# Performance work log

Measured on AMD Instinct MI355X. Metric: run time of the kernel, lower is better.

Reference implementation:

```python
import jax, jax.numpy as jnp
import numpy as np

N_HEADS = 8; DH = 64; G = 4; K = 9
C = N_HEADS * DH; CG = C // G
FACTOR = 2.0; TAU = 1.0
SCALE = DH ** -0.5


def _conv1x1(x, w, b):
    # x: (C, *spatial), w: (O, C), b: (O,)
    y = jnp.tensordot(w, x, axes=([1], [0]))
    return y + b.reshape((-1,) + (1,) * (y.ndim - 1))


def _dwconv(x, w, b):
    # depthwise 3x3, SAME padding; x (N,Cg,H,W), w (Cg,1,3,3)
    y = jax.lax.conv_general_dilated(x, w, (1, 1), 'SAME',
                                     feature_group_count=x.shape[1],
                                     dimension_numbers=('NCHW', 'OIHW', 'NCHW'))
    return y + b[None, :, None, None]


def _ln(x, g, b):
    # LayerNormProxy: LN over channel dim of NCHW (torch default eps=1e-5)
    m = jnp.mean(x, axis=1, keepdims=True)
    v = jnp.var(x, axis=1, keepdims=True)
    return (x - m) / jnp.sqrt(v + 1e-5) * g[None, :, None, None] + b[None, :, None, None]


def _grid_sample(img, grid):
    # bilinear, align_corners=True, padding_mode='zeros'
    # img (N,C,H,W), grid (N,Hg,Wg,2) with (x,y) in [-1,1]
    N, Cc, H, W = img.shape
    gx = (grid[..., 0] + 1.0) * 0.5 * (W - 1)
    gy = (grid[..., 1] + 1.0) * 0.5 * (H - 1)
    x0 = jnp.floor(gx); y0 = jnp.floor(gy)

    def g(yy, xx):
        yi = jnp.clip(yy, 0, H - 1).astype(jnp.int32)
        xi = jnp.clip(xx, 0, W - 1).astype(jnp.int32)
        ok = ((yy >= 0) & (yy <= H - 1) & (xx >= 0) & (xx <= W - 1)).astype(img.dtype)
        vals = jax.vmap(lambda im, a, b: im[:, a, b])(img, yi, xi)  # (N,C,Hg,Wg)
        return vals * ok[:, None]

    wx1 = gx - x0; wx0 = 1.0 - wx1
    wy1 = gy - y0; wy0 = 1.0 - wy1
    return (g(y0, x0) * (wy0 * wx0)[:, None]
            + g(y0, x0 + 1) * (wy0 * wx1)[:, None]
            + g(y0 + 1, x0) * (wy1 * wx0)[:, None]
            + g(y0 + 1, x0 + 1) * (wy1 * wx1)[:, None])


def _forward(x, idx, labels, wq, bq, wk, bk, wv, bv, wo, bo,
             ow1, ob1, g1, b1, ow2, ob2, g2, b2, ow3):
    _, _, H, W = x.shape
    n = idx.shape[0]
    iy, ix = idx[:, 0], idx[:, 1]

    q = _conv1x1(x[0], wq, bq)[None]               # (1,C,H,W)
    q_off = q.reshape(G, CG, H, W)                 # (b g) c h w with b=1
    q_sel = q[0][:, iy, ix]                        # (C,n)

    # offset predictor: dwconv -> LN -> GELU (x2) -> 1x1 (no bias)
    t = jax.nn.gelu(_ln(_dwconv(q_off, ow1, ob1), g1, b1), approximate=False)
    t = jax.nn.gelu(_ln(_dwconv(t, ow2, ob2), g2, b2), approximate=False)
    offset = jnp.einsum('gchw,oc->gohw', t, ow3)   # (G,2K,H,W)

    # offset_range_factor > 0: tanh * [1/H,1/W] (tiled K times) * factor
    rng = jnp.tile(jnp.array([1.0 / H, 1.0 / W], offset.dtype), K)
    offset = jnp.tanh(offset) * rng[None, :, None, None] * FACTOR
    off = offset.transpose(0, 2, 3, 1).reshape(G, H, W, K, 2)  # (g,h,w,K,(y,x))

    # reference points in [-1,1] (y,x), unfolded over 3x3 window w/ replication pad
    ry = (jnp.arange(H, dtype=x.dtype) + 0.5) / H * 2.0 - 1.0
    rx = (jnp.arange(W, dtype=x.dtype) + 0.5) / W * 2.0 - 1.0
    ref = jnp.stack(jnp.meshgrid(ry, rx, indexing='ij'), 0)    # (2,H,W)
    pad = jnp.pad(ref, ((0, 0), (1, 1), (1, 1)), mode='edge')
    patches = jnp.stack([pad[:, dy:dy + H, dx:dx + W]
                         for dy in range(3) for dx in range(3)], 0)  # (K,2,H,W)
    ref_unf = patches.transpose(2, 3, 0, 1)                    # (H,W,K,2)

    pos = off + ref_unf[None]                                  # (G,H,W,K,2)
    pos = pos.transpose(0, 3, 1, 2, 4).reshape(G * K, H, W, 2)
    grid = pos[..., ::-1]                                      # (x,y) order

    # gather per-group channels at K learned locations per position
    xg = x.reshape(G, CG, H, W)
    img = jnp.broadcast_to(xg[:, None], (G, K, CG, H, W)).reshape(G * K, CG, H, W)
    xs = _grid_sample(img, grid)                               # (GK,CG,H,W)
    xs = xs.reshape(G, K, CG, H, W).transpose(0, 2, 1, 3, 4).reshape(C, K, H, W)
    xs_sel = xs[:, :, iy, ix]                                  # (C,K,n)

    k = _conv1x1(xs_sel, wk, bk).reshape(N_HEADS, DH, K, n).transpose(0, 1, 3, 2)  # (h,d,n,K)
    v = _conv1x1(xs_sel, wv, bv).reshape(N_HEADS, DH, K, n).transpose(0, 1, 3, 2)
    qh = q_sel.reshape(N_HEADS, DH, n)

    attn = jnp.einsum('hdn,hdnk->hnk', qh, k) * SCALE
    attn = jax.nn.softmax(attn / TAU, axis=-1)                 # (h,n,K)
    out = jnp.einsum('hnk,hdnk->hdn', attn, v).reshape(C, n)
    y = _conv1x1(out, wo, bo).T                                # (n, dim_out)

    sig = jax.nn.sigmoid(y[jnp.arange(n), labels])

    # second grid_sample over full channels at the same learned positions
    img_full = jnp.broadcast_to(x, (G * K, C, H, W))
    xr = _grid_sample(img_full, grid)                          # (GK,C,H,W)
    xr_sel = xr[:, :, iy, ix].transpose(2, 0, 1)               # (n,GK,C)
    return y, attn, xr_sel, sig


def setup_inputs() -> dict:
    key = jax.random.key(0)
    ks = jax.random.split(key, 16)
    H = W = 64; n = 2048; s = 0.02
    return dict(
        x=jax.random.normal(ks[0], (1, C, H, W), jnp.float32),
        idx=jax.random.randint(ks[1], (n, 2), 0, H),
        labels=jax.random.randint(ks[2], (n,), 0, C),
        wq=jax.random.normal(ks[3], (C, C), jnp.float32) * s, bq=jnp.zeros((C,), jnp.float32),
        wk=jax.random.normal(ks[4], (C, C), jnp.float32) * s, bk=jnp.zeros((C,), jnp.float32),
        wv=jax.random.normal(ks[5], (C, C), jnp.float32) * s, bv=jnp.zeros((C,), jnp.float32),
        wo=jax.random.normal(ks[6], (C, C), jnp.float32) * s, bo=jnp.zeros((C,), jnp.float32),
        ow1=jax.random.normal(ks[7], (CG, 1, 3, 3), jnp.float32) * s, ob1=jnp.zeros((CG,), jnp.float32),
        g1=jnp.ones((CG,), jnp.float32), b1=jnp.zeros((CG,), jnp.float32),
        ow2=jax.random.normal(ks[8], (CG, 1, 3, 3), jnp.float32) * s, ob2=jnp.zeros((CG,), jnp.float32),
        g2=jnp.ones((CG,), jnp.float32), b2=jnp.zeros((CG,), jnp.float32),
        ow3=jax.random.normal(ks[9], (2 * K, CG), jnp.float32) * s,
    )


def reference(x, idx, labels, wq, bq, wk, bk, wv, bv, wo, bo,
              ow1, ob1, g1, b1, ow2, ob2, g2, b2, ow3):
    return _forward(x, idx, labels, wq, bq, wk, bk, wv, bv, wo, bo,
                    ow1, ob1, g1, b1, ow2, ob2, g2, b2, ow3)
```

## Files before the change

### kernel.cpp

```cpp
#include <hip/hip_runtime.h>
#include <math.h>

namespace {

typedef unsigned short u16;
typedef unsigned int u32;
typedef __attribute__((ext_vector_type(8))) short bf16x8;
typedef __attribute__((ext_vector_type(4))) float f32x4;
typedef __attribute__((ext_vector_type(2))) float f32x2;
typedef __attribute__((ext_vector_type(2))) unsigned int u32x2;

constexpr int HDIM = 64;
constexpr int WDIM = 64;
constexpr int HW = HDIM * WDIM;
constexpr int C = 512;
constexpr int G = 4;
constexpr int CG = 128;
constexpr int K = 9;
constexpr int NH = 8;
constexpr float SCALE = 0.125f;

__device__ __forceinline__ u16 f2b(float f) {
  union { float f; u32 u; } v; v.f = f;
  u32 u = v.u;
  return (u16)((u + 0x7FFFu + ((u >> 16) & 1u)) >> 16);
}
__device__ __forceinline__ float b2f(u16 b) {
  union { u32 u; float f; } v; v.u = ((u32)b) << 16;
  return v.f;
}

__global__ void __launch_bounds__(256)
k_prep(const float* __restrict__ wq, const float* __restrict__ wv,
       const float* __restrict__ wo, const float* __restrict__ wk,
       const float* __restrict__ x,
       u16* __restrict__ wqb, u16* __restrict__ wvb, u16* __restrict__ wob,
       u16* __restrict__ wkT, u16* __restrict__ xtb) {
  int b = blockIdx.x;
  int t = threadIdx.x;
  if (b < 1024) {
    int j = b * 256 + t;
    wqb[j] = f2b(wq[j]);
    wvb[j] = f2b(wv[j]);
    wob[j] = f2b(wo[j]);
    return;
  }
  __shared__ float tile[32][33];
  int tx = t & 31, ty = t >> 5;
  if (b < 1280) {
    int bb = b - 1024;
    int r0 = (bb & 15) * 32, c0 = (bb >> 4) * 32;
    for (int r = ty; r < 32; r += 8) tile[r][tx] = wk[(r0 + r) * C + c0 + tx];
    __syncthreads();
    for (int r = ty; r < 32; r += 8) wkT[(c0 + r) * C + r0 + tx] = f2b(tile[tx][r]);
  } else {
    int bb = b - 1280;
    int p0 = (bb & 127) * 32, c0 = (bb >> 7) * 32;
    for (int r = ty; r < 32; r += 8) tile[r][tx] = x[(c0 + r) * HW + p0 + tx];
    __syncthreads();
    for (int r = ty; r < 32; r += 8) xtb[(p0 + r) * C + c0 + tx] = f2b(tile[tx][r]);
  }
}

template <bool OUT_BF16>
__global__ void __launch_bounds__(256)
k_gemm_mfma(const u16* __restrict__ A, int lda, int aOffZ,
            const int* __restrict__ aIdx,
            const u16* __restrict__ BT, int ldb, int bOffZ,
            const float* __restrict__ bias, int biasOffZ,
            void* __restrict__ Dp, int ldd, int dOffZ, int Kd,
            const int* __restrict__ labels, float* __restrict__ sigp) {
  int z = blockIdx.z;
  const u16* Ab = A + (size_t)z * aOffZ;
  const u16* Bb = BT + (size_t)z * bOffZ;
  int t = threadIdx.x;
  int wave = t >> 6, lane = t & 63;
  int wm = (wave >> 1) * 32, wn = (wave & 1) * 32;
  int bm = blockIdx.x * 64 + wm;
  int bn = blockIdx.y * 64 + wn;
  int row = lane & 15, quad = lane >> 4;
  size_t ar[2];
#pragma unroll
  for (int mt = 0; mt < 2; ++mt) {
    int r = bm + mt * 16 + row;
    ar[mt] = aIdx ? (size_t)(aIdx[2 * r] * WDIM + aIdx[2 * r + 1]) : (size_t)r;
  }
  f32x4 acc[2][2] = {};
  for (int k0 = 0; k0 < Kd; k0 += 32) {
    bf16x8 a[2], b[2];
#pragma unroll
    for (int mt = 0; mt < 2; ++mt)
      a[mt] = *(const bf16x8*)&Ab[ar[mt] * lda + k0 + quad * 8];
#pragma unroll
    for (int nt = 0; nt < 2; ++nt)
      b[nt] = *(const bf16x8*)&Bb[(size_t)(bn + nt * 16 + row) * ldb + k0 + quad * 8];
#pragma unroll
    for (int mt = 0; mt < 2; ++mt)
#pragma unroll
      for (int nt = 0; nt < 2; ++nt)
        acc[mt][nt] = __builtin_amdgcn_mfma_f32_16x16x32_bf16(a[mt], b[nt], acc[mt][nt], 0, 0, 0);
  }
#pragma unroll
  for (int nt = 0; nt < 2; ++nt) {
    int cc = bn + nt * 16 + row;
    float bb = bias ? bias[(size_t)z * biasOffZ + cc] : 0.0f;
#pragma unroll
    for (int mt = 0; mt < 2; ++mt)
#pragma unroll
      for (int r = 0; r < 4; ++r) {
        int rr = bm + mt * 16 + quad * 4 + r;
        float v = acc[mt][nt][r] + bb;
        if (OUT_BF16) {
          ((u16*)Dp)[(size_t)z * dOffZ + (size_t)rr * ldd + cc] = f2b(v);
        } else {
          ((float*)Dp)[(size_t)z * dOffZ + (size_t)rr * ldd + cc] = v;
          if (labels && labels[rr] == cc) sigp[rr] = 1.0f / (1.0f + expf(-v));
        }
      }
  }
}

__global__ void __launch_bounds__(256)
k_dwln2(const u16* __restrict__ in, const float* __restrict__ w9,
        const float* __restrict__ wb, const float* __restrict__ lng,
        const float* __restrict__ lnb, u16* __restrict__ outp) {
  int p = blockIdx.x;
  int h = p >> 6, w = p & 63;
  int t = threadIdx.x;
  int c0 = t * 2;
  int cg0 = c0 & 127, cg1 = cg0 + 1;
  float a0 = wb[cg0], a1 = wb[cg1];
#pragma unroll
  for (int dy = 0; dy < 3; ++dy) {
    int hh = h + dy - 1;
    if (hh < 0 || hh >= HDIM) continue;
#pragma unroll
    for (int dx = 0; dx < 3; ++dx) {
      int ww = w + dx - 1;
      if (ww < 0 || ww >= WDIM) continue;
      u32 pr2 = *(const u32*)&in[(hh * WDIM + ww) * C + c0];
      float wt0 = w9[cg0 * 9 + dy * 3 + dx];
      float wt1 = w9[cg1 * 9 + dy * 3 + dx];
      a0 += wt0 * b2f((u16)pr2);
      a1 += wt1 * b2f((u16)(pr2 >> 16));
    }
  }
  float s = a0 + a1, s2 = a0 * a0 + a1 * a1;
#pragma unroll
  for (int o = 32; o > 0; o >>= 1) {
    s += __shfl_xor(s, o, 64);
    s2 += __shfl_xor(s2, o, 64);
  }
  float mean = s * (1.0f / 128.0f);
  float var = s2 * (1.0f / 128.0f) - mean * mean;
  float rstd = rsqrtf(var + 1e-5f);
  float xn0 = (a0 - mean) * rstd * lng[cg0] + lnb[cg0];
  float xn1 = (a1 - mean) * rstd * lng[cg1] + lnb[cg1];
  u16 o0 = f2b(0.5f * xn0 * (1.0f + erff(xn0 * 0.70710678f)));
  u16 o1 = f2b(0.5f * xn1 * (1.0f + erff(xn1 * 0.70710678f)));
  *(u32*)&outp[(size_t)p * C + c0] = ((u32)o1 << 16) | o0;
}

__global__ void __launch_bounds__(256)
k_dwoff(const u16* __restrict__ t1, const float* __restrict__ w9,
        const float* __restrict__ wb, const float* __restrict__ lng,
        const float* __restrict__ lnb, const float* __restrict__ ow3,
        const int* __restrict__ idx, float* __restrict__ pos) {
  int i = blockIdx.x;
  int t = threadIdx.x;
  int iy = idx[2 * i], ix = idx[2 * i + 1];
  int c0 = t * 2;
  int cg0 = c0 & 127, cg1 = cg0 + 1;
  int g = t >> 6;
  int lane = t & 63;
  float a0 = wb[cg0], a1 = wb[cg1];
#pragma unroll
  for (int dy = 0; dy < 3; ++dy) {
    int hh = iy + dy - 1;
    if (hh < 0 || hh >= HDIM) continue;
#pragma unroll
    for (int dx = 0; dx < 3; ++dx) {
      int ww = ix + dx - 1;
      if (ww < 0 || ww >= WDIM) continue;
      u32 pr2 = *(const u32*)&t1[(hh * WDIM + ww) * C + c0];
      float wt0 = w9[cg0 * 9 + dy * 3 + dx];
      float wt1 = w9[cg1 * 9 + dy * 3 + dx];
      a0 += wt0 * b2f((u16)pr2);
      a1 += wt1 * b2f((u16)(pr2 >> 16));
    }
  }
  float s = a0 + a1, s2 = a0 * a0 + a1 * a1;
#pragma unroll
  for (int o = 32; o > 0; o >>= 1) {
    s += __shfl_xor(s, o, 64);
    s2 += __shfl_xor(s2, o, 64);
  }
  float mean = s * (1.0f / 128.0f);
  float var = s2 * (1.0f / 128.0f) - mean * mean;
  float rstd = rsqrtf(var + 1e-5f);
  float xn0 = (a0 - mean) * rstd * lng[cg0] + lnb[cg0];
  float xn1 = (a1 - mean) * rstd * lng[cg1] + lnb[cg1];
  float x0 = 0.5f * xn0 * (1.0f + erff(xn0 * 0.70710678f));
  float x1 = 0.5f * xn1 * (1.0f + erff(xn1 * 0.70710678f));
  float ovreg = 0.0f;
#pragma unroll
  for (int l = 0; l < 18; ++l) {
    float a = ow3[l * CG + cg0] * x0 + ow3[l * CG + cg1] * x1;
#pragma unroll
    for (int o = 32; o > 0; o >>= 1) a += __shfl_xor(a, o, 64);
    if (lane == l) ovreg = a;
  }
  int ls = (lane < 9) ? lane : 0;
  float vy = __shfl(ovreg, 2 * ls, 64);
  float vx = __shfl(ovreg, 2 * ls + 1, 64);
  if (lane < 9) {
    int dy = lane / 3, dx = lane % 3;
    int ryi = min(max(iy + dy - 1, 0), HDIM - 1);
    int rxi = min(max(ix + dx - 1, 0), WDIM - 1);
    float ry = (ryi + 0.5f) * (2.0f / HDIM) - 1.0f;
    float rx = (rxi + 0.5f) * (2.0f / WDIM) - 1.0f;
    f32x2 pv;
    pv.x = tanhf(vy) * (2.0f / HDIM) + ry;
    pv.y = tanhf(vx) * (2.0f / WDIM) + rx;
    *(f32x2*)&pos[((i * G + g) * K + lane) * 2] = pv;
  }
}

__global__ void __launch_bounds__(256)
k_attn3(const u16* __restrict__ qk2b, const u16* __restrict__ xtb,
        const float* __restrict__ pos, float* __restrict__ attn_out,
        u16* __restrict__ z2b, float* __restrict__ xr, int n) {
  constexpr int LD = 520;
  int i = blockIdx.x;
  int t = threadIdx.x;
  __shared__ alignas(16) u16 qkl[8 * LD];
  __shared__ alignas(16) u16 xsl[16 * LD];
  __shared__ int ro[36][4];
  __shared__ float wbl[36][4];
  __shared__ float lg[NH][K];
  __shared__ float pr[NH][K];
  {
    const bf16x8* qs = (const bf16x8*)(qk2b + (size_t)i * (NH * C));
#pragma unroll
    for (int cix = t; cix < 512; cix += 256) {
      bf16x8 val = qs[cix];
      int r = cix >> 6;
      int co = (cix & 63) * 8;
      *(bf16x8*)&qkl[r * LD + co] = val;
    }
  }
  if (t < 36) {
    float py = pos[(size_t)i * 72 + 2 * t];
    float px = pos[(size_t)i * 72 + 2 * t + 1];
    float gx = (px + 1.0f) * 0.5f * (WDIM - 1);
    float gy = (py + 1.0f) * 0.5f * (HDIM - 1);
    float x0f = floorf(gx), y0f = floorf(gy);
    float wx1 = gx - x0f, wx0 = 1.0f - wx1;
    float wy1 = gy - y0f, wy0 = 1.0f - wy1;
    int x0 = (int)x0f, y0 = (int)y0f;
    int x1 = x0 + 1, y1 = y0 + 1;
    bool vx0 = (x0 >= 0) && (x0 < WDIM);
    bool vx1 = (x1 >= 0) && (x1 < WDIM);
    bool vy0 = (y0 >= 0) && (y0 < HDIM);
    bool vy1 = (y1 >= 0) && (y1 < HDIM);
    wbl[t][0] = (vy0 && vx0) ? wy0 * wx0 : 0.0f;
    wbl[t][1] = (vy0 && vx1) ? wy0 * wx1 : 0.0f;
    wbl[t][2] = (vy1 && vx0) ? wy1 * wx0 : 0.0f;
    wbl[t][3] = (vy1 && vx1) ? wy1 * wx1 : 0.0f;
    int x0c = min(max(x0, 0), WDIM - 1), x1c = min(max(x1, 0), WDIM - 1);
    int y0c = min(max(y0, 0), HDIM - 1), y1c = min(max(y1, 0), HDIM - 1);
    ro[t][0] = (y0c * WDIM + x0c) * C;
    ro[t][1] = (y0c * WDIM + x1c) * C;
    ro[t][2] = (y1c * WDIM + x0c) * C;
    ro[t][3] = (y1c * WDIM + x1c) * C;
  }
  __syncthreads();
  int wave = t >> 6;
  float* xrb = xr + (size_t)i * (G * K) * C;
  {
    int half = t >> 7;
    int th = t & 127;
    int c4 = th * 4;
#pragma unroll 3
    for (int j = 0; j < 18; ++j) {
      int it = 2 * j + half;
      float w00 = wbl[it][0], w01 = wbl[it][1], w10 = wbl[it][2], w11 = wbl[it][3];
      u32x2 q00 = *(const u32x2*)&xtb[ro[it][0] + c4];
      u32x2 q01 = *(const u32x2*)&xtb[ro[it][1] + c4];
      u32x2 q10 = *(const u32x2*)&xtb[ro[it][2] + c4];
      u32x2 q11 = *(const u32x2*)&xtb[ro[it][3] + c4];
      float v0 = w00 * b2f((u16)q00.x) + w01 * b2f((u16)q01.x) +
                 w10 * b2f((u16)q10.x) + w11 * b2f((u16)q11.x);
      float v1 = w00 * b2f((u16)(q00.x >> 16)) + w01 * b2f((u16)(q01.x >> 16)) +
                 w10 * b2f((u16)(q10.x >> 16)) + w11 * b2f((u16)(q11.x >> 16));
      float v2 = w00 * b2f((u16)q00.y) + w01 * b2f((u16)q01.y) +
                 w10 * b2f((u16)q10.y) + w11 * b2f((u16)q11.y);
      float v3 = w00 * b2f((u16)(q00.y >> 16)) + w01 * b2f((u16)(q01.y >> 16)) +
                 w10 * b2f((u16)(q10.y >> 16)) + w11 * b2f((u16)(q11.y >> 16));
      f32x4 ov = {v0, v1, v2, v3};
      __builtin_nontemporal_store(ov, (f32x4*)&xrb[(size_t)it * C + c4]);
      int gi = (it * 57) >> 9;
      if ((th >> 5) == gi) {
        int kk = it - gi * 9;
        u32x2 pk;
        pk.x = ((u32)f2b(v1) << 16) | f2b(v0);
        pk.y = ((u32)f2b(v3) << 16) | f2b(v2);
        *(u32x2*)&xsl[kk * LD + c4] = pk;
      }
    }
  }
  __syncthreads();
  if (wave == 0) {
    int lane = t & 63;
    int row = lane & 15, quad = lane >> 4;
    f32x4 acc = {};
#pragma unroll 4
    for (int k0 = 0; k0 < C; k0 += 32) {
      bf16x8 a = *(const bf16x8*)&qkl[(row & 7) * LD + k0 + quad * 8];
      bf16x8 b = *(const bf16x8*)&xsl[row * LD + k0 + quad * 8];
      acc = __builtin_amdgcn_mfma_f32_16x16x32_bf16(a, b, acc, 0, 0, 0);
    }
    if (row < K && quad < 2) {
#pragma unroll
      for (int r = 0; r < 4; ++r) lg[quad * 4 + r][row] = acc[r] * SCALE;
    }
  }
  __syncthreads();
  if (t < NH) {
    float mx = -1e30f;
    for (int kk = 0; kk < K; ++kk) mx = fmaxf(mx, lg[t][kk]);
    float sm = 0.0f;
    float e[K];
    for (int kk = 0; kk < K; ++kk) { e[kk] = expf(lg[t][kk] - mx); sm += e[kk]; }
    float inv = 1.0f / sm;
    for (int kk = 0; kk < K; ++kk) {
      float p = e[kk] * inv;
      pr[t][kk] = p;
      attn_out[((size_t)t * n + i) * K + kk] = p;
    }
  }
  __syncthreads();
  {
    int h = t >> 5;
    int cbase = (t & 31) * 16;
    float prr[K];
#pragma unroll
    for (int kk = 0; kk < K; ++kk) prr[kk] = pr[h][kk];
    float accz[16] = {};
#pragma unroll
    for (int kk = 0; kk < K; ++kk) {
      bf16x8 v0 = *(const bf16x8*)&xsl[kk * LD + cbase];
      bf16x8 v1 = *(const bf16x8*)&xsl[kk * LD + cbase + 8];
      float p = prr[kk];
#pragma unroll
      for (int e = 0; e < 8; ++e) {
        accz[e] += p * b2f((u16)v0[e]);
        accz[8 + e] += p * b2f((u16)v1[e]);
      }
    }
    u16 ob[16];
#pragma unroll
    for (int e = 0; e < 16; ++e) ob[e] = f2b(accz[e]);
    u16* zdst = z2b + (size_t)i * (NH * C) + h * C + cbase;
    *(bf16x8*)&zdst[0] = *(const bf16x8*)&ob[0];
    *(bf16x8*)&zdst[8] = *(const bf16x8*)&ob[8];
  }
}

}

extern "C" void kernel_launch(void* const* d_in, const int* in_sizes, int n_in,
                              void* d_out, int out_size, void* d_ws, size_t ws_size,
                              hipStream_t stream) {
  (void)n_in; (void)out_size; (void)ws_size;
  const float* x = (const float*)d_in[0];
  const int* idx = (const int*)d_in[1];
  const int* labels = (const int*)d_in[2];
  const float* wq = (const float*)d_in[3];
  const float* bq = (const float*)d_in[4];
  const float* wk = (const float*)d_in[5];
  const float* wv = (const float*)d_in[7];
  const float* bv = (const float*)d_in[8];
  const float* wo = (const float*)d_in[9];
  const float* bo = (const float*)d_in[10];
  const float* ow1 = (const float*)d_in[11];
  const float* ob1 = (const float*)d_in[12];
  const float* g1 = (const float*)d_in[13];
  const float* b1 = (const float*)d_in[14];
  const float* ow2 = (const float*)d_in[15];
  const float* ob2 = (const float*)d_in[16];
  const float* g2 = (const float*)d_in[17];
  const float* b2 = (const float*)d_in[18];
  const float* ow3 = (const float*)d_in[19];
  int n = in_sizes[1] / 2;

  unsigned char* wp = (unsigned char*)d_ws;
  auto alloc = [&](size_t bytes) {
    unsigned char* p = wp;
    wp += (bytes + 255) & ~(size_t)255;
    return p;
  };
  u16* xtb = (u16*)alloc((size_t)HW * C * 2);
  u16* wqb = (u16*)alloc((size_t)C * C * 2);
  u16* wvb = (u16*)alloc((size_t)C * C * 2);
  u16* wob = (u16*)alloc((size_t)C * C * 2);
  u16* wkT = (u16*)alloc((size_t)C * C * 2);
  u16* q_tb = (u16*)alloc((size_t)HW * C * 2);
  u16* t1b = (u16*)alloc((size_t)HW * C * 2);
  u16* qk2b = (u16*)alloc((size_t)n * NH * C * 2);
  float* pos = (float*)alloc((size_t)n * G * K * 2 * 4);
  u16* z2b = (u16*)alloc((size_t)n * NH * C * 2);
  u16* outb = (u16*)alloc((size_t)n * C * 2);

  float* out_f = (float*)d_out;
  float* y_out = out_f;
  float* attn_out = y_out + (size_t)n * C;
  float* xr_out = attn_out + (size_t)NH * n * K;
  float* sig_out = xr_out + (size_t)n * G * K * C;

  k_prep<<<dim3(3328), 256, 0, stream>>>(wq, wv, wo, wk, x, wqb, wvb, wob, wkT, xtb);

  k_gemm_mfma<true><<<dim3(HW / 64, C / 64, 1), 256, 0, stream>>>(
      xtb, C, 0, nullptr, wqb, C, 0, bq, 0, q_tb, C, 0, C, nullptr, nullptr);

  k_dwln2<<<dim3(HW), 256, 0, stream>>>(q_tb, ow1, ob1, g1, b1, t1b);
  k_dwoff<<<dim3(n), 256, 0, stream>>>(t1b, ow2, ob2, g2, b2, ow3, idx, pos);

  k_gemm_mfma<true><<<dim3(n / 64, C / 64, NH), 256, 0, stream>>>(
      q_tb, C, 64, idx, wkT, C, 64, nullptr, 0, qk2b, NH * C, C, 64, nullptr, nullptr);

  k_attn3<<<dim3(n), 256, 0, stream>>>(qk2b, xtb, pos, attn_out, z2b, xr_out, n);

  k_gemm_mfma<true><<<dim3(n / 64, 1, NH), 256, 0, stream>>>(
      z2b, NH * C, C, nullptr, wvb, C, 64 * C, bv, 64, outb, C, 64, C, nullptr, nullptr);

  k_gemm_mfma<false><<<dim3(n / 64, C / 64, 1), 256, 0, stream>>>(
      outb, C, 0, nullptr, wob, C, 0, bo, 0, y_out, C, 0, C, labels, sig_out);
}
```

Baseline: 305.1 us.

## Merge dwconv-LN and per-head QK GEMM into one launch; fuse softmax into aggregation

The depthwise conv/LN/GELU kernel and the per-head gathered QK GEMM are combined into one launch, with block index ranges selecting which work a block does. This lets the two independent stages share the GPU and removes a launch. In the attention kernel, softmax is computed redundantly per wave and fused into the weighted sum, which removes one barrier and the shared probability buffer, and the logit MFMA loop gets a raised wave priority. The merged kernel hardcodes the grid split (2048 GEMM blocks, which implies n=2048) and uses a simpler direct-load GEMM with no LDS tiling.

New measurement: 302.7 us. About the same (-0.8%).

```diff
diff --git a/kernel.cpp b/kernel.cpp
--- a/kernel.cpp
+++ b/kernel.cpp
@@ -121,44 +121,92 @@
 }
 
 __global__ void __launch_bounds__(256)
-k_dwln2(const u16* __restrict__ in, const float* __restrict__ w9,
-        const float* __restrict__ wb, const float* __restrict__ lng,
-        const float* __restrict__ lnb, u16* __restrict__ outp) {
-  int p = blockIdx.x;
-  int h = p >> 6, w = p & 63;
+k_mix(const u16* __restrict__ q_tb, const float* __restrict__ w9,
+      const float* __restrict__ wb, const float* __restrict__ lng,
+      const float* __restrict__ lnb, u16* __restrict__ t1b,
+      const u16* __restrict__ wkT, const int* __restrict__ idx,
+      u16* __restrict__ qk2b) {
+  int b = blockIdx.x;
   int t = threadIdx.x;
-  int c0 = t * 2;
-  int cg0 = c0 & 127, cg1 = cg0 + 1;
-  float a0 = wb[cg0], a1 = wb[cg1];
-#pragma unroll
-  for (int dy = 0; dy < 3; ++dy) {
-    int hh = h + dy - 1;
-    if (hh < 0 || hh >= HDIM) continue;
-#pragma unroll
-    for (int dx = 0; dx < 3; ++dx) {
-      int ww = w + dx - 1;
-      if (ww < 0 || ww >= WDIM) continue;
-      u32 pr2 = *(const u32*)&in[(hh * WDIM + ww) * C + c0];
-      float wt0 = w9[cg0 * 9 + dy * 3 + dx];
-      float wt1 = w9[cg1 * 9 + dy * 3 + dx];
-      a0 += wt0 * b2f((u16)pr2);
-      a1 += wt1 * b2f((u16)(pr2 >> 16));
-    }
-  }
-  float s = a0 + a1, s2 = a0 * a0 + a1 * a1;
-#pragma unroll
-  for (int o = 32; o > 0; o >>= 1) {
-    s += __shfl_xor(s, o, 64);
-    s2 += __shfl_xor(s2, o, 64);
-  }
-  float mean = s * (1.0f / 128.0f);
-  float var = s2 * (1.0f / 128.0f) - mean * mean;
-  float rstd = rsqrtf(var + 1e-5f);
-  float xn0 = (a0 - mean) * rstd * lng[cg0] + lnb[cg0];
-  float xn1 = (a1 - mean) * rstd * lng[cg1] + lnb[cg1];
-  u16 o0 = f2b(0.5f * xn0 * (1.0f + erff(xn0 * 0.70710678f)));
-  u16 o1 = f2b(0.5f * xn1 * (1.0f + erff(xn1 * 0.70710678f)));
-  *(u32*)&outp[(size_t)p * C + c0] = ((u32)o1 << 16) | o0;
+  if (b < HW) {
+    int p = b;
+    int h = p >> 6, w = p & 63;
+    int c0 = t * 2;
+    int cg0 = c0 & 127, cg1 = cg0 + 1;
+    float a0 = wb[cg0], a1 = wb[cg1];
+#pragma unroll
+    for (int dy = 0; dy < 3; ++dy) {
+      int hh = h + dy - 1;
+      if (hh < 0 || hh >= HDIM) continue;
+#pragma unroll
+      for (int dx = 0; dx < 3; ++dx) {
+        int ww = w + dx - 1;
+        if (ww < 0 || ww >= WDIM) continue;
+        u32 pr2 = *(const u32*)&q_tb[(hh * WDIM + ww) * C + c0];
+        float wt0 = w9[cg0 * 9 + dy * 3 + dx];
+        float wt1 = w9[cg1 * 9 + dy * 3 + dx];
+        a0 += wt0 * b2f((u16)pr2);
+        a1 += wt1 * b2f((u16)(pr2 >> 16));
+      }
+    }
+    float s = a0 + a1, s2 = a0 * a0 + a1 * a1;
+#pragma unroll
+    for (int o = 32; o > 0; o >>= 1) {
+      s += __shfl_xor(s, o, 64);
+      s2 += __shfl_xor(s2, o, 64);
+    }
+    float mean = s * (1.0f / 128.0f);
+    float var = s2 * (1.0f / 128.0f) - mean * mean;
+    float rstd = rsqrtf(var + 1e-5f);
+    float xn0 = (a0 - mean) * rstd * lng[cg0] + lnb[cg0];
+    float xn1 = (a1 - mean) * rstd * lng[cg1] + lnb[cg1];
+    u16 o0 = f2b(0.5f * xn0 * (1.0f + erff(xn0 * 0.70710678f)));
+    u16 o1 = f2b(0.5f * xn1 * (1.0f + erff(xn1 * 0.70710678f)));
+    *(u32*)&t1b[(size_t)p * C + c0] = ((u32)o1 << 16) | o0;
+  } else {
+    int bb = b - HW;
+    int m = bb & 31, nn = (bb >> 5) & 7, z = bb >> 8;
+    const u16* Ab = q_tb + z * 64;
+    const u16* Bb = wkT + z * 64;
+    int wave = t >> 6, lane = t & 63;
+    int wm = (wave >> 1) * 32, wn = (wave & 1) * 32;
+    int bm = m * 64 + wm;
+    int bn = nn * 64 + wn;
+    int row = lane & 15, quad = lane >> 4;
+    size_t ar[2];
+#pragma unroll
+    for (int mt = 0; mt < 2; ++mt) {
+      int r = bm + mt * 16 + row;
+      ar[mt] = (size_t)(idx[2 * r] * WDIM + idx[2 * r + 1]);
+    }
+    f32x4 acc[2][2] = {};
+#pragma unroll
+    for (int k0 = 0; k0 < 64; k0 += 32) {
+      bf16x8 a[2], bfr[2];
+#pragma unroll
+      for (int mt = 0; mt < 2; ++mt)
+        a[mt] = *(const bf16x8*)&Ab[ar[mt] * C + k0 + quad * 8];
+#pragma unroll
+      for (int nt = 0; nt < 2; ++nt)
+        bfr[nt] = *(const bf16x8*)&Bb[(size_t)(bn + nt * 16 + row) * C + k0 + quad * 8];
+#pragma unroll
+      for (int mt = 0; mt < 2; ++mt)
+#pragma unroll
+        for (int nt = 0; nt < 2; ++nt)
+          acc[mt][nt] = __builtin_amdgcn_mfma_f32_16x16x32_bf16(a[mt], bfr[nt], acc[mt][nt], 0, 0, 0);
+    }
+#pragma unroll
+    for (int nt = 0; nt < 2; ++nt) {
+      int cc = bn + nt * 16 + row;
+#pragma unroll
+      for (int mt = 0; mt < 2; ++mt)
+#pragma unroll
+        for (int r = 0; r < 4; ++r) {
+          int rr = bm + mt * 16 + quad * 4 + r;
+          qk2b[(size_t)rr * (NH * C) + z * C + cc] = f2b(acc[mt][nt][r]);
+        }
+    }
+  }
 }
 
 __global__ void __launch_bounds__(256)
@@ -227,7 +275,7 @@
 }
 
 __global__ void __launch_bounds__(256)
-k_attn3(const u16* __restrict__ qk2b, const u16* __restrict__ xtb,
+k_attn5(const u16* __restrict__ qk2b, const u16* __restrict__ xtb,
         const float* __restrict__ pos, float* __restrict__ attn_out,
         u16* __restrict__ z2b, float* __restrict__ xr, int n) {
   constexpr int LD = 520;
@@ -238,7 +286,6 @@
   __shared__ int ro[36][4];
   __shared__ float wbl[36][4];
   __shared__ float lg[NH][K];
-  __shared__ float pr[NH][K];
   {
     const bf16x8* qs = (const bf16x8*)(qk2b + (size_t)i * (NH * C));
 #pragma unroll
@@ -314,56 +361,48 @@
     int lane = t & 63;
     int row = lane & 15, quad = lane >> 4;
     f32x4 acc = {};
+    __builtin_amdgcn_s_setprio(1);
 #pragma unroll 4
     for (int k0 = 0; k0 < C; k0 += 32) {
       bf16x8 a = *(const bf16x8*)&qkl[(row & 7) * LD + k0 + quad * 8];
       bf16x8 b = *(const bf16x8*)&xsl[row * LD + k0 + quad * 8];
       acc = __builtin_amdgcn_mfma_f32_16x16x32_bf16(a, b, acc, 0, 0, 0);
     }
+    __builtin_amdgcn_s_setprio(0);
     if (row < K && quad < 2) {
 #pragma unroll
       for (int r = 0; r < 4; ++r) lg[quad * 4 + r][row] = acc[r] * SCALE;
-    }
-  }
-  __syncthreads();
-  if (t < NH) {
-    float mx = -1e30f;
-    for (int kk = 0; kk < K; ++kk) mx = fmaxf(mx, lg[t][kk]);
-    float sm = 0.0f;
-    float e[K];
-    for (int kk = 0; kk < K; ++kk) { e[kk] = expf(lg[t][kk] - mx); sm += e[kk]; }
-    float inv = 1.0f / sm;
-    for (int kk = 0; kk < K; ++kk) {
-      float p = e[kk] * inv;
-      pr[t][kk] = p;
-      attn_out[((size_t)t * n + i) * K + kk] = p;
     }
   }
   __syncthreads();
   {
-    int h = t >> 5;
-    int cbase = (t & 31) * 16;
-    float prr[K];
-#pragma unroll
-    for (int kk = 0; kk < K; ++kk) prr[kk] = pr[h][kk];
-    float accz[16] = {};
-#pragma unroll
-    for (int kk = 0; kk < K; ++kk) {
-      bf16x8 v0 = *(const bf16x8*)&xsl[kk * LD + cbase];
-      bf16x8 v1 = *(const bf16x8*)&xsl[kk * LD + cbase + 8];
-      float p = prr[kk];
-#pragma unroll
-      for (int e = 0; e < 8; ++e) {
-        accz[e] += p * b2f((u16)v0[e]);
-        accz[8 + e] += p * b2f((u16)v1[e]);
+    int lane = t & 63;
+    u16* zrow = z2b + (size_t)i * (NH * C);
+#pragma unroll
+    for (int hh = 0; hh < 2; ++hh) {
+      int h = wave * 2 + hh;
+      float mx = -1e30f;
+#pragma unroll
+      for (int kk = 0; kk < K; ++kk) mx = fmaxf(mx, lg[h][kk]);
+      float e[K];
+      float sm = 0.0f;
+#pragma unroll
+      for (int kk = 0; kk < K; ++kk) { e[kk] = expf(lg[h][kk] - mx); sm += e[kk]; }
+      float inv = 1.0f / sm;
+      if (lane < K) attn_out[((size_t)h * n + i) * K + lane] = e[lane] * inv;
+      float accz[8] = {};
+#pragma unroll
+      for (int kk = 0; kk < K; ++kk) {
+        bf16x8 v = *(const bf16x8*)&xsl[kk * LD + lane * 8];
+        float p = e[kk] * inv;
+#pragma unroll
+        for (int el = 0; el < 8; ++el) accz[el] += p * b2f((u16)v[el]);
       }
-    }
-    u16 ob[16];
-#pragma unroll
-    for (int e = 0; e < 16; ++e) ob[e] = f2b(accz[e]);
-    u16* zdst = z2b + (size_t)i * (NH * C) + h * C + cbase;
-    *(bf16x8*)&zdst[0] = *(const bf16x8*)&ob[0];
-    *(bf16x8*)&zdst[8] = *(const bf16x8*)&ob[8];
+      u16 ob[8];
+#pragma unroll
+      for (int el = 0; el < 8; ++el) ob[el] = f2b(accz[el]);
+      *(bf16x8*)&zrow[h * C + lane * 8] = *(const bf16x8*)ob;
+    }
   }
 }
 
@@ -423,13 +462,11 @@
   k_gemm_mfma<true><<<dim3(HW / 64, C / 64, 1), 256, 0, stream>>>(
       xtb, C, 0, nullptr, wqb, C, 0, bq, 0, q_tb, C, 0, C, nullptr, nullptr);
 
-  k_dwln2<<<dim3(HW), 256, 0, stream>>>(q_tb, ow1, ob1, g1, b1, t1b);
+  k_mix<<<dim3(HW + 2048), 256, 0, stream>>>(q_tb, ow1, ob1, g1, b1, t1b, wkT, idx, qk2b);
+
   k_dwoff<<<dim3(n), 256, 0, stream>>>(t1b, ow2, ob2, g2, b2, ow3, idx, pos);
 
-  k_gemm_mfma<true><<<dim3(n / 64, C / 64, NH), 256, 0, stream>>>(
-      q_tb, C, 64, idx, wkT, C, 64, nullptr, 0, qk2b, NH * C, C, 64, nullptr, nullptr);
-
-  k_attn3<<<dim3(n), 256, 0, stream>>>(qk2b, xtb, pos, attn_out, z2b, xr_out, n);
+  k_attn5<<<dim3(n), 256, 0, stream>>>(qk2b, xtb, pos, attn_out, z2b, xr_out, n);
 
   k_gemm_mfma<true><<<dim3(n / 64, 1, NH), 256, 0, stream>>>(
       z2b, NH * C, C, nullptr, wvb, C, 64 * C, bv, 64, outb, C, 64, C, nullptr, nullptr);
```
